# Optimization experiments

Measured on AMD Instinct MI355X. Metric: run time of the kernel, lower is better.

The kernel has to match this reference:

```python
import jax, jax.numpy as jnp
import numpy as np

B, H, M, DH = 8, 32, 8, 64  # batch, spatial h=w, heads, dim_head
C = M * DH
HW = H * H


def _make_pos_idx(h: int) -> np.ndarray:
    # A[i, j] = j - i, matching tf.constant([range(i, i+h) for i in range(0, -h, -1)])
    A = np.arange(h)[None, :] - np.arange(h)[:, None]
    horiz = np.tile(A, (h, h))                              # (h^2, h^2)
    vert = np.repeat(np.repeat(A, h, axis=0), h, axis=1)    # (h^2, h^2)
    return (2 * h - 1) * (vert + h - 1) + (horiz + h - 1)   # values in [0, (2h-1)^2)


def setup_inputs() -> dict:
    key = jax.random.key(0)
    ks = jax.random.split(key, 4)
    x = jax.random.normal(ks[0], (B, H, H, C), dtype=jnp.float32)
    w_qkv = jax.random.normal(ks[1], (DH, 3 * DH), dtype=jnp.float32) * (1.0 / np.sqrt(DH))
    b_qkv = jnp.zeros((3 * DH,), dtype=jnp.float32)
    w_ht = jax.random.normal(ks[2], (C, C), dtype=jnp.float32) * (1.0 / np.sqrt(C))
    b_ht = jnp.zeros((C,), dtype=jnp.float32)
    # Glorot-normal scalar table over (2h-1)^2 relative positions
    n_rel = (2 * H - 1) ** 2
    pos_table = jax.random.normal(ks[3], (n_rel,), dtype=jnp.float32) * np.float32(np.sqrt(2.0 / (n_rel + 1)))
    pos_idx = jnp.asarray(_make_pos_idx(H), dtype=jnp.int32)  # (HW, HW)
    return {"x": x, "w_qkv": w_qkv, "b_qkv": b_qkv, "w_ht": w_ht, "b_ht": b_ht,
            "pos_table": pos_table, "pos_idx": pos_idx}


def reference(x, w_qkv, b_qkv, w_ht, b_ht, pos_table, pos_idx):
    b, h, w, c = x.shape
    d_h = c // M
    # split heads into the batch dim: (b*M, h, w, d_h)
    xh = x.reshape(b, h, w, M, d_h).transpose(0, 3, 1, 2, 4).reshape(b * M, h, w, d_h)
    # 1x1 conv == per-pixel dense
    qkv = xh @ w_qkv + b_qkv                       # (b*M, h, w, 3*DH)
    qkv = qkv.reshape(b * M, h * w, DH, 3)
    q, k, v = qkv[..., 0], qkv[..., 1], qkv[..., 2]
    q = q / jnp.sqrt(jnp.float32(DH))
    att = jnp.einsum('bic,bjc->bij', q, k)         # (b*M, HW, HW)
    pos_emb = pos_table[pos_idx]                   # (HW, HW) gathered bias
    att = jax.nn.softmax(att + pos_emb, axis=-1)
    o = jnp.einsum('bij,bjc->bic', att, v)         # (b*M, HW, DH)
    o = o.reshape(b, M, h, w, d_h).transpose(0, 2, 3, 1, 4).reshape(b, h, w, c)
    out = o @ w_ht + b_ht                          # 1x1 head_transform conv
    return (out, att, pos_emb)
```

## Files before the change

kernel.cpp:

```cpp
#include <hip/hip_runtime.h>
#include <hip/hip_bf16.h>

typedef __attribute__((ext_vector_type(8))) __bf16 bf16x8;
typedef __attribute__((ext_vector_type(8))) short  s16x8;
typedef __attribute__((ext_vector_type(4))) short  s16x4;
typedef __attribute__((ext_vector_type(4))) float  f32x4;

#define HW2 1024
#define CDIM 512

static __device__ __forceinline__ unsigned short f2b(float f) {
  __hip_bfloat16 h = __float2bfloat16(f);
  return __builtin_bit_cast(unsigned short, h);
}

static __device__ __forceinline__ f32x4 mfma16(s16x8 a, s16x8 b, f32x4 c) {
  return __builtin_amdgcn_mfma_f32_16x16x32_bf16(
      __builtin_bit_cast(bf16x8, a), __builtin_bit_cast(bf16x8, b), c, 0, 0, 0);
}

static __device__ __forceinline__ void lds_fence() {
  asm volatile("s_waitcnt lgkmcnt(0)" ::: "memory");
  __builtin_amdgcn_sched_barrier(0);
}

__global__ __launch_bounds__(256) void k_prep(
    const float* __restrict__ w_qkv, const float* __restrict__ w_ht,
    const float* __restrict__ table, const int* __restrict__ idx,
    unsigned short* __restrict__ Wtq, unsigned short* __restrict__ Wtk,
    unsigned short* __restrict__ Wtv, unsigned short* __restrict__ WhtT,
    float* __restrict__ pe) {
  int blk = blockIdx.x;
  if (blk < 16) {
    int i = blk * 256 + threadIdx.x;
    int c = i >> 6, k = i & 63;
    const float* src = w_qkv + k * 192 + 3 * c;
    Wtq[i] = f2b(src[0] * 0.125f);
    Wtk[i] = f2b(src[1]);
    Wtv[i] = f2b(src[2]);
  } else if (blk < 1040) {
    int i = (blk - 16) * 256 + threadIdx.x;
    int c = i >> 9, k = i & 511;
    WhtT[i] = f2b(w_ht[k * 512 + c]);
  } else {
    int i = (blk - 1040) * 256 + threadIdx.x;
    #pragma unroll
    for (int j = 0; j < 4; ++j) {
      int p = i + j * 262144;
      pe[p] = table[idx[p]];
    }
  }
}

__global__ __launch_bounds__(256) void k_qkv(const float* __restrict__ x,
    const float* __restrict__ b_qkv,
    const unsigned short* __restrict__ Wtq, const unsigned short* __restrict__ Wtk,
    const unsigned short* __restrict__ Wtv,
    unsigned short* __restrict__ Qb, unsigned short* __restrict__ Kb,
    unsigned short* __restrict__ Vt) {
  int bm = blockIdx.x >> 4;
  int pt = blockIdx.x & 15;
  int wid = threadIdx.x >> 6, lane = threadIdx.x & 63;
  int l15 = lane & 15, lg = lane >> 4;
  int b = bm >> 3, m = bm & 7;
  int pbase = pt * 64 + wid * 16;

  int pA = pbase + l15;
  const float* xp = x + (size_t)(b * HW2 + pA) * CDIM + m * 64 + lg * 8;
  f32x4 xv0 = *(const f32x4*)(xp);
  f32x4 xv1 = *(const f32x4*)(xp + 4);
  f32x4 xv2 = *(const f32x4*)(xp + 32);
  f32x4 xv3 = *(const f32x4*)(xp + 36);
  s16x8 a0, a1;
  #pragma unroll
  for (int j = 0; j < 4; ++j) {
    a0[j]     = (short)f2b(xv0[j]);
    a0[4 + j] = (short)f2b(xv1[j]);
    a1[j]     = (short)f2b(xv2[j]);
    a1[4 + j] = (short)f2b(xv3[j]);
  }

  f32x4 acc[12];
  #pragma unroll
  for (int ct = 0; ct < 12; ++ct) acc[ct] = (f32x4){0.f, 0.f, 0.f, 0.f};

  #pragma unroll
  for (int ct = 0; ct < 12; ++ct) {
    const unsigned short* W = (ct < 4) ? Wtq : (ct < 8 ? Wtk : Wtv);
    int c = (ct & 3) * 16 + l15;
    const unsigned short* wp = W + c * 64 + lg * 8;
    s16x8 b0 = *(const s16x8*)(wp);
    s16x8 b1 = *(const s16x8*)(wp + 32);
    if (ct < 8) {
      acc[ct] = mfma16(b0, a0, acc[ct]);
      acc[ct] = mfma16(b1, a1, acc[ct]);
    } else {
      acc[ct] = mfma16(a0, b0, acc[ct]);
      acc[ct] = mfma16(a1, b1, acc[ct]);
    }
  }

  #pragma unroll
  for (int ct = 0; ct < 8; ++ct) {
    int s = ct >> 2;
    int c0 = (ct & 3) * 16 + lg * 4;
    unsigned short* D = (s == 0) ? Qb : Kb;
    s16x4 pk;
    #pragma unroll
    for (int i = 0; i < 4; ++i) {
      float bias = b_qkv[3 * (c0 + i) + s];
      if (s == 0) bias *= 0.125f;
      pk[i] = (short)f2b(acc[ct][i] + bias);
    }
    *(s16x4*)(D + (size_t)(bm * HW2 + pbase + l15) * 64 + c0) = pk;
  }
  #pragma unroll
  for (int ct = 8; ct < 12; ++ct) {
    int c = (ct & 3) * 16 + l15;
    float bias = b_qkv[3 * c + 2];
    s16x4 pk;
    #pragma unroll
    for (int i = 0; i < 4; ++i) pk[i] = (short)f2b(acc[ct][i] + bias);
    *(s16x4*)(Vt + ((size_t)bm * 64 + c) * HW2 + pbase + lg * 4) = pk;
  }
}

__global__ __launch_bounds__(256, 4) void k_attn(
    const unsigned short* __restrict__ Qb, const unsigned short* __restrict__ Kb,
    const unsigned short* __restrict__ Vt, const float* __restrict__ ptab,
    float* __restrict__ att, unsigned short* __restrict__ O) {
  int r8 = blockIdx.x & 7;
  int kk = blockIdx.x >> 3;
  int qt = kk & 63;
  int bm = ((kk >> 6) << 3) | r8;
  int wid = threadIdx.x >> 6, lane = threadIdx.x & 63;
  int l15 = lane & 15, lg = lane >> 4;

  __shared__ __align__(16) unsigned char buf[16 * 1032 * 2];
  __shared__ float redm[4][16];
  __shared__ float reds[4][16];
  unsigned short (*P)[1032] = (unsigned short(*)[1032])buf;

  const unsigned short* qp = Qb + (size_t)(bm * HW2 + qt * 16 + l15) * 64 + lg * 8;
  s16x8 qa0 = *(const s16x8*)qp;
  s16x8 qa1 = *(const s16x8*)(qp + 32);

  f32x4 acc[16];
  const unsigned short* kbase = Kb + (size_t)bm * HW2 * 64;
  #pragma unroll
  for (int ct = 0; ct < 16; ++ct) {
    int col = wid * 256 + ct * 16 + l15;
    const unsigned short* kp = kbase + (size_t)col * 64 + lg * 8;
    s16x8 kb0 = *(const s16x8*)kp;
    s16x8 kb1 = *(const s16x8*)(kp + 32);
    f32x4 a = (f32x4){0.f, 0.f, 0.f, 0.f};
    a = mfma16(kb0, qa0, a);
    a = mfma16(kb1, qa1, a);
    acc[ct] = a;
  }

  int cb = 1984 - 63 * (qt >> 1) - ((qt & 1) << 4) - l15;
  float pm = -1e30f;
  #pragma unroll
  for (int ct = 0; ct < 16; ++ct) {
    int c0 = wid * 256 + ct * 16 + lg * 4;
    int t0 = 63 * (c0 >> 5) + (c0 & 31) + cb;
    f32x4 pv;
    __builtin_memcpy(&pv, ptab + t0, 16);
    #pragma unroll
    for (int i = 0; i < 4; ++i) {
      float v = acc[ct][i] + pv[i];
      acc[ct][i] = v;
      pm = fmaxf(pm, v);
    }
  }
  pm = fmaxf(pm, __shfl_xor(pm, 16));
  pm = fmaxf(pm, __shfl_xor(pm, 32));
  if (lane < 16) redm[wid][l15] = pm;
  __syncthreads();
  float mrow = fmaxf(fmaxf(redm[0][l15], redm[1][l15]),
                     fmaxf(redm[2][l15], redm[3][l15]));

  float ps = 0.f;
  #pragma unroll
  for (int ct = 0; ct < 16; ++ct) {
    #pragma unroll
    for (int i = 0; i < 4; ++i) {
      float e = __expf(acc[ct][i] - mrow);
      acc[ct][i] = e;
      ps += e;
    }
  }
  ps += __shfl_xor(ps, 16);
  ps += __shfl_xor(ps, 32);
  if (lane < 16) reds[wid][l15] = ps;
  __syncthreads();
  float inv = 1.0f / (reds[0][l15] + reds[1][l15] + reds[2][l15] + reds[3][l15]);

  #pragma unroll
  for (int ct = 0; ct < 16; ++ct) {
    int c0 = wid * 256 + ct * 16 + lg * 4;
    s16x4 pk;
    #pragma unroll
    for (int i = 0; i < 4; ++i) {
      float v = acc[ct][i] * inv;
      acc[ct][i] = v;
      pk[i] = (short)f2b(v);
    }
    *(s16x4*)&P[l15][c0] = pk;
  }
  __syncthreads();

  f32x4 o = (f32x4){0.f, 0.f, 0.f, 0.f};
  const unsigned short* vbase = Vt + (size_t)(bm * 64 + wid * 16 + l15) * HW2;
  #pragma unroll
  for (int kt = 0; kt < 32; ++kt) {
    s16x8 vb = *(const s16x8*)(vbase + kt * 32 + lg * 8);
    s16x8 pa = *(const s16x8*)&P[l15][kt * 32 + lg * 8];
    o = mfma16(vb, pa, o);
  }
  s16x4 ok;
  #pragma unroll
  for (int i = 0; i < 4; ++i) ok[i] = (short)f2b(o[i]);
  *(s16x4*)(O + (size_t)(bm * HW2 + qt * 16 + l15) * 64 + wid * 16 + lg * 4) = ok;

  __syncthreads();

  float* stgw = (float*)buf + wid * 1024;
  float* abase = att + (size_t)(bm * HW2 + qt * 16) * HW2 + wid * 256;
  #pragma unroll
  for (int q = 0; q < 4; ++q) {
    #pragma unroll
    for (int t4 = 0; t4 < 4; ++t4) {
      int ct = q * 4 + t4;
      f32x4 vv;
      #pragma unroll
      for (int i = 0; i < 4; ++i) vv[i] = acc[ct][i];
      int cw = (t4 * 4 + lg) ^ (l15 & 7);
      *(f32x4*)&stgw[l15 * 64 + cw * 4] = vv;
    }
    lds_fence();
    f32x4 vals[4];
    #pragma unroll
    for (int i = 0; i < 4; ++i) {
      int r = i * 4 + lg;
      int cr = l15 ^ (r & 7);
      vals[i] = *(const f32x4*)&stgw[r * 64 + cr * 4];
    }
    lds_fence();
    #pragma unroll
    for (int i = 0; i < 4; ++i) {
      int r = i * 4 + lg;
      __builtin_nontemporal_store(vals[i],
          (f32x4*)(abase + (size_t)r * HW2 + q * 64 + l15 * 4));
    }
  }
}

__global__ __launch_bounds__(256) void k_ht(
    const unsigned short* __restrict__ O, const unsigned short* __restrict__ WhtT,
    const float* __restrict__ b_ht, float* __restrict__ out) {
  int rt = blockIdx.x >> 1;
  int ch = blockIdx.x & 1;
  int wid = threadIdx.x >> 6, lane = threadIdx.x & 63;
  int wr = wid >> 1, wc = wid & 1;
  int l15 = lane & 15, lg = lane >> 4;
  int b = (rt * 32) >> 10;
  int p0 = (rt * 32) & 1023;

  __shared__ unsigned short A[32][520];

  int t = threadIdx.x;
  #pragma unroll
  for (int j = 0; j < 8; ++j) {
    int idx = t * 8 + j * 2048;
    int row = idx >> 9;
    int k0 = idx & 511;
    int m = k0 >> 6, kk = k0 & 63;
    const unsigned short* src = O + (size_t)((b * 8 + m) * HW2 + p0 + row) * 64 + kk;
    *(s16x8*)&A[row][k0] = *(const s16x8*)src;
  }
  __syncthreads();

  f32x4 acc[8];
  #pragma unroll
  for (int ct = 0; ct < 8; ++ct) acc[ct] = (f32x4){0.f, 0.f, 0.f, 0.f};

  #pragma unroll
  for (int kt = 0; kt < 16; ++kt) {
    s16x8 a = *(const s16x8*)&A[wr * 16 + l15][kt * 32 + lg * 8];
    #pragma unroll
    for (int ct = 0; ct < 8; ++ct) {
      int col = ch * 256 + wc * 128 + ct * 16 + l15;
      s16x8 bf = *(const s16x8*)(WhtT + (size_t)col * 512 + kt * 32 + lg * 8);
      acc[ct] = mfma16(bf, a, acc[ct]);
    }
  }

  int rp = rt * 32 + wr * 16 + l15;
  #pragma unroll
  for (int ct = 0; ct < 8; ++ct) {
    int c0 = ch * 256 + wc * 128 + ct * 16 + lg * 4;
    f32x4 bb = *(const f32x4*)(b_ht + c0);
    f32x4 ov;
    #pragma unroll
    for (int i = 0; i < 4; ++i) ov[i] = acc[ct][i] + bb[i];
    *(f32x4*)(out + (size_t)rp * 512 + c0) = ov;
  }
}

extern "C" void kernel_launch(void* const* d_in, const int* in_sizes, int n_in,
                              void* d_out, int out_size, void* d_ws, size_t ws_size,
                              hipStream_t stream) {
  const float* x         = (const float*)d_in[0];
  const float* w_qkv     = (const float*)d_in[1];
  const float* b_qkv     = (const float*)d_in[2];
  const float* w_ht      = (const float*)d_in[3];
  const float* b_ht      = (const float*)d_in[4];
  const float* pos_table = (const float*)d_in[5];
  const int*   pos_idx   = (const int*)d_in[6];

  float* out = (float*)d_out;
  float* att = out + 4194304;
  float* pe  = att + 67108864;

  char* ws = (char*)d_ws;
  unsigned short* Qb   = (unsigned short*)(ws);
  unsigned short* Kb   = (unsigned short*)(ws + (8u  << 20));
  unsigned short* Vt   = (unsigned short*)(ws + (16u << 20));
  unsigned short* O    = (unsigned short*)(ws + (24u << 20));
  unsigned short* Wtq  = (unsigned short*)(ws + (32u << 20));
  unsigned short* Wtk  = Wtq + 4096;
  unsigned short* Wtv  = Wtk + 4096;
  unsigned short* WhtT = (unsigned short*)(ws + (32u << 20) + 65536);

  k_prep<<<2064, 256, 0, stream>>>(w_qkv, w_ht, pos_table, pos_idx,
                                   Wtq, Wtk, Wtv, WhtT, pe);
  k_qkv <<<1024, 256, 0, stream>>>(x, b_qkv, Wtq, Wtk, Wtv, Qb, Kb, Vt);
  k_attn<<<4096, 256, 0, stream>>>(Qb, Kb, Vt, pos_table, att, O);
  k_ht  <<<512,  256, 0, stream>>>(O, WhtT, b_ht, out);
}
```

Measured before the change: 203.9 us.

## Fuse attention and head-transform into one kernel with per-wave heads and two-pass softmax

```diff
diff --git a/kernel.cpp b/kernel.cpp
--- a/kernel.cpp
+++ b/kernel.cpp
@@ -125,187 +125,175 @@
   }
 }
 
-__global__ __launch_bounds__(256, 4) void k_attn(
+__global__ __launch_bounds__(512, 4) void k_fused(
     const unsigned short* __restrict__ Qb, const unsigned short* __restrict__ Kb,
     const unsigned short* __restrict__ Vt, const float* __restrict__ ptab,
-    float* __restrict__ att, unsigned short* __restrict__ O) {
-  int r8 = blockIdx.x & 7;
-  int kk = blockIdx.x >> 3;
-  int qt = kk & 63;
-  int bm = ((kk >> 6) << 3) | r8;
+    const unsigned short* __restrict__ WhtT, const float* __restrict__ b_ht,
+    float* __restrict__ att, float* __restrict__ out) {
+  int b  = blockIdx.x & 7;
+  int qt = blockIdx.x >> 3;
   int wid = threadIdx.x >> 6, lane = threadIdx.x & 63;
   int l15 = lane & 15, lg = lane >> 4;
-
-  __shared__ __align__(16) unsigned char buf[16 * 1032 * 2];
-  __shared__ float redm[4][16];
-  __shared__ float reds[4][16];
-  unsigned short (*P)[1032] = (unsigned short(*)[1032])buf;
+  int bm = b * 8 + wid;
+
+  __shared__ __align__(16) unsigned char wbuf[8][4352];
+  __shared__ unsigned short Osm[16][520];
 
   const unsigned short* qp = Qb + (size_t)(bm * HW2 + qt * 16 + l15) * 64 + lg * 8;
   s16x8 qa0 = *(const s16x8*)qp;
   s16x8 qa1 = *(const s16x8*)(qp + 32);
-
-  f32x4 acc[16];
   const unsigned short* kbase = Kb + (size_t)bm * HW2 * 64;
-  #pragma unroll
-  for (int ct = 0; ct < 16; ++ct) {
-    int col = wid * 256 + ct * 16 + l15;
-    const unsigned short* kp = kbase + (size_t)col * 64 + lg * 8;
-    s16x8 kb0 = *(const s16x8*)kp;
-    s16x8 kb1 = *(const s16x8*)(kp + 32);
-    f32x4 a = (f32x4){0.f, 0.f, 0.f, 0.f};
-    a = mfma16(kb0, qa0, a);
-    a = mfma16(kb1, qa1, a);
-    acc[ct] = a;
-  }
-
   int cb = 1984 - 63 * (qt >> 1) - ((qt & 1) << 4) - l15;
-  float pm = -1e30f;
-  #pragma unroll
-  for (int ct = 0; ct < 16; ++ct) {
-    int c0 = wid * 256 + ct * 16 + lg * 4;
-    int t0 = 63 * (c0 >> 5) + (c0 & 31) + cb;
-    f32x4 pv;
-    __builtin_memcpy(&pv, ptab + t0, 16);
-    #pragma unroll
-    for (int i = 0; i < 4; ++i) {
-      float v = acc[ct][i] + pv[i];
-      acc[ct][i] = v;
-      pm = fmaxf(pm, v);
-    }
-  }
-  pm = fmaxf(pm, __shfl_xor(pm, 16));
-  pm = fmaxf(pm, __shfl_xor(pm, 32));
-  if (lane < 16) redm[wid][l15] = pm;
+
+  float mrow = -1e30f, srow = 0.f;
+  for (int ch = 0; ch < 8; ++ch) {
+    f32x4 acc[8];
+    #pragma unroll
+    for (int ct = 0; ct < 8; ++ct) {
+      int col = ch * 128 + ct * 16 + l15;
+      const unsigned short* kp = kbase + (size_t)col * 64 + lg * 8;
+      s16x8 kb0 = *(const s16x8*)kp;
+      s16x8 kb1 = *(const s16x8*)(kp + 32);
+      f32x4 a = (f32x4){0.f, 0.f, 0.f, 0.f};
+      a = mfma16(kb0, qa0, a);
+      a = mfma16(kb1, qa1, a);
+      acc[ct] = a;
+    }
+    float cm = -1e30f;
+    #pragma unroll
+    for (int ct = 0; ct < 8; ++ct) {
+      int c0 = ch * 128 + ct * 16 + lg * 4;
+      int t0 = 63 * (c0 >> 5) + (c0 & 31) + cb;
+      f32x4 pv;
+      __builtin_memcpy(&pv, ptab + t0, 16);
+      #pragma unroll
+      for (int i = 0; i < 4; ++i) {
+        float v = acc[ct][i] + pv[i];
+        acc[ct][i] = v;
+        cm = fmaxf(cm, v);
+      }
+    }
+    cm = fmaxf(cm, __shfl_xor(cm, 16));
+    cm = fmaxf(cm, __shfl_xor(cm, 32));
+    float mn = fmaxf(mrow, cm);
+    float cs = 0.f;
+    #pragma unroll
+    for (int ct = 0; ct < 8; ++ct)
+      #pragma unroll
+      for (int i = 0; i < 4; ++i) cs += __expf(acc[ct][i] - mn);
+    cs += __shfl_xor(cs, 16);
+    cs += __shfl_xor(cs, 32);
+    srow = srow * __expf(mrow - mn) + cs;
+    mrow = mn;
+  }
+  float inv = 1.0f / srow;
+
+  float* stgw = (float*)&wbuf[wid][0];
+  unsigned short* Pw = (unsigned short*)&wbuf[wid][0];
+  float* abase = att + (size_t)(bm * HW2 + qt * 16) * HW2;
+  f32x4 o[4];
+  #pragma unroll
+  for (int d = 0; d < 4; ++d) o[d] = (f32x4){0.f, 0.f, 0.f, 0.f};
+
+  for (int ch = 0; ch < 8; ++ch) {
+    f32x4 acc[8];
+    #pragma unroll
+    for (int ct = 0; ct < 8; ++ct) {
+      int col = ch * 128 + ct * 16 + l15;
+      const unsigned short* kp = kbase + (size_t)col * 64 + lg * 8;
+      s16x8 kb0 = *(const s16x8*)kp;
+      s16x8 kb1 = *(const s16x8*)(kp + 32);
+      f32x4 a = (f32x4){0.f, 0.f, 0.f, 0.f};
+      a = mfma16(kb0, qa0, a);
+      a = mfma16(kb1, qa1, a);
+      acc[ct] = a;
+    }
+    #pragma unroll
+    for (int ct = 0; ct < 8; ++ct) {
+      int c0 = ch * 128 + ct * 16 + lg * 4;
+      int t0 = 63 * (c0 >> 5) + (c0 & 31) + cb;
+      f32x4 pv;
+      __builtin_memcpy(&pv, ptab + t0, 16);
+      #pragma unroll
+      for (int i = 0; i < 4; ++i)
+        acc[ct][i] = __expf(acc[ct][i] + pv[i] - mrow) * inv;
+    }
+    #pragma unroll
+    for (int q = 0; q < 2; ++q) {
+      #pragma unroll
+      for (int t4 = 0; t4 < 4; ++t4) {
+        int cw = (t4 * 4 + lg) ^ (l15 & 7);
+        *(f32x4*)&stgw[l15 * 64 + cw * 4] = acc[q * 4 + t4];
+      }
+      lds_fence();
+      f32x4 vals[4];
+      #pragma unroll
+      for (int i = 0; i < 4; ++i) {
+        int r = i * 4 + lg;
+        int cr = l15 ^ (r & 7);
+        vals[i] = *(const f32x4*)&stgw[r * 64 + cr * 4];
+      }
+      lds_fence();
+      #pragma unroll
+      for (int i = 0; i < 4; ++i) {
+        int r = i * 4 + lg;
+        __builtin_nontemporal_store(vals[i],
+            (f32x4*)(abase + (size_t)r * HW2 + ch * 128 + q * 64 + l15 * 4));
+      }
+    }
+    #pragma unroll
+    for (int ct = 0; ct < 8; ++ct) {
+      int c = ct * 16 + lg * 4;
+      s16x4 pk;
+      #pragma unroll
+      for (int i = 0; i < 4; ++i) pk[i] = (short)f2b(acc[ct][i]);
+      *(s16x4*)&Pw[l15 * 136 + c] = pk;
+    }
+    lds_fence();
+    #pragma unroll
+    for (int d = 0; d < 4; ++d) {
+      const unsigned short* vp =
+          Vt + (size_t)(bm * 64 + d * 16 + l15) * HW2 + ch * 128;
+      #pragma unroll
+      for (int kt = 0; kt < 4; ++kt) {
+        s16x8 vb = *(const s16x8*)(vp + kt * 32 + lg * 8);
+        s16x8 pa = *(const s16x8*)&Pw[l15 * 136 + kt * 32 + lg * 8];
+        o[d] = mfma16(vb, pa, o[d]);
+      }
+    }
+    lds_fence();
+  }
+
+  #pragma unroll
+  for (int d = 0; d < 4; ++d) {
+    s16x4 ok;
+    #pragma unroll
+    for (int i = 0; i < 4; ++i) ok[i] = (short)f2b(o[d][i]);
+    *(s16x4*)&Osm[l15][wid * 64 + d * 16 + lg * 4] = ok;
+  }
   __syncthreads();
-  float mrow = fmaxf(fmaxf(redm[0][l15], redm[1][l15]),
-                     fmaxf(redm[2][l15], redm[3][l15]));
-
-  float ps = 0.f;
-  #pragma unroll
-  for (int ct = 0; ct < 16; ++ct) {
-    #pragma unroll
-    for (int i = 0; i < 4; ++i) {
-      float e = __expf(acc[ct][i] - mrow);
-      acc[ct][i] = e;
-      ps += e;
-    }
-  }
-  ps += __shfl_xor(ps, 16);
-  ps += __shfl_xor(ps, 32);
-  if (lane < 16) reds[wid][l15] = ps;
-  __syncthreads();
-  float inv = 1.0f / (reds[0][l15] + reds[1][l15] + reds[2][l15] + reds[3][l15]);
-
-  #pragma unroll
-  for (int ct = 0; ct < 16; ++ct) {
-    int c0 = wid * 256 + ct * 16 + lg * 4;
-    s16x4 pk;
-    #pragma unroll
-    for (int i = 0; i < 4; ++i) {
-      float v = acc[ct][i] * inv;
-      acc[ct][i] = v;
-      pk[i] = (short)f2b(v);
-    }
-    *(s16x4*)&P[l15][c0] = pk;
-  }
-  __syncthreads();
-
-  f32x4 o = (f32x4){0.f, 0.f, 0.f, 0.f};
-  const unsigned short* vbase = Vt + (size_t)(bm * 64 + wid * 16 + l15) * HW2;
-  #pragma unroll
-  for (int kt = 0; kt < 32; ++kt) {
-    s16x8 vb = *(const s16x8*)(vbase + kt * 32 + lg * 8);
-    s16x8 pa = *(const s16x8*)&P[l15][kt * 32 + lg * 8];
-    o = mfma16(vb, pa, o);
-  }
-  s16x4 ok;
-  #pragma unroll
-  for (int i = 0; i < 4; ++i) ok[i] = (short)f2b(o[i]);
-  *(s16x4*)(O + (size_t)(bm * HW2 + qt * 16 + l15) * 64 + wid * 16 + lg * 4) = ok;
-
-  __syncthreads();
-
-  float* stgw = (float*)buf + wid * 1024;
-  float* abase = att + (size_t)(bm * HW2 + qt * 16) * HW2 + wid * 256;
-  #pragma unroll
-  for (int q = 0; q < 4; ++q) {
-    #pragma unroll
-    for (int t4 = 0; t4 < 4; ++t4) {
-      int ct = q * 4 + t4;
-      f32x4 vv;
-      #pragma unroll
-      for (int i = 0; i < 4; ++i) vv[i] = acc[ct][i];
-      int cw = (t4 * 4 + lg) ^ (l15 & 7);
-      *(f32x4*)&stgw[l15 * 64 + cw * 4] = vv;
-    }
-    lds_fence();
-    f32x4 vals[4];
-    #pragma unroll
-    for (int i = 0; i < 4; ++i) {
-      int r = i * 4 + lg;
-      int cr = l15 ^ (r & 7);
-      vals[i] = *(const f32x4*)&stgw[r * 64 + cr * 4];
-    }
-    lds_fence();
-    #pragma unroll
-    for (int i = 0; i < 4; ++i) {
-      int r = i * 4 + lg;
-      __builtin_nontemporal_store(vals[i],
-          (f32x4*)(abase + (size_t)r * HW2 + q * 64 + l15 * 4));
-    }
-  }
-}
-
-__global__ __launch_bounds__(256) void k_ht(
-    const unsigned short* __restrict__ O, const unsigned short* __restrict__ WhtT,
-    const float* __restrict__ b_ht, float* __restrict__ out) {
-  int rt = blockIdx.x >> 1;
-  int ch = blockIdx.x & 1;
-  int wid = threadIdx.x >> 6, lane = threadIdx.x & 63;
-  int wr = wid >> 1, wc = wid & 1;
-  int l15 = lane & 15, lg = lane >> 4;
-  int b = (rt * 32) >> 10;
-  int p0 = (rt * 32) & 1023;
-
-  __shared__ unsigned short A[32][520];
-
-  int t = threadIdx.x;
-  #pragma unroll
-  for (int j = 0; j < 8; ++j) {
-    int idx = t * 8 + j * 2048;
-    int row = idx >> 9;
-    int k0 = idx & 511;
-    int m = k0 >> 6, kk = k0 & 63;
-    const unsigned short* src = O + (size_t)((b * 8 + m) * HW2 + p0 + row) * 64 + kk;
-    *(s16x8*)&A[row][k0] = *(const s16x8*)src;
-  }
-  __syncthreads();
-
-  f32x4 acc[8];
-  #pragma unroll
-  for (int ct = 0; ct < 8; ++ct) acc[ct] = (f32x4){0.f, 0.f, 0.f, 0.f};
-
+
+  f32x4 ah[4];
+  #pragma unroll
+  for (int ct = 0; ct < 4; ++ct) ah[ct] = (f32x4){0.f, 0.f, 0.f, 0.f};
   #pragma unroll
   for (int kt = 0; kt < 16; ++kt) {
-    s16x8 a = *(const s16x8*)&A[wr * 16 + l15][kt * 32 + lg * 8];
-    #pragma unroll
-    for (int ct = 0; ct < 8; ++ct) {
-      int col = ch * 256 + wc * 128 + ct * 16 + l15;
+    s16x8 oa = *(const s16x8*)&Osm[l15][kt * 32 + lg * 8];
+    #pragma unroll
+    for (int ct = 0; ct < 4; ++ct) {
+      int col = wid * 64 + ct * 16 + l15;
       s16x8 bf = *(const s16x8*)(WhtT + (size_t)col * 512 + kt * 32 + lg * 8);
-      acc[ct] = mfma16(bf, a, acc[ct]);
-    }
-  }
-
-  int rp = rt * 32 + wr * 16 + l15;
-  #pragma unroll
-  for (int ct = 0; ct < 8; ++ct) {
-    int c0 = ch * 256 + wc * 128 + ct * 16 + lg * 4;
+      ah[ct] = mfma16(bf, oa, ah[ct]);
+    }
+  }
+  #pragma unroll
+  for (int ct = 0; ct < 4; ++ct) {
+    int c0 = wid * 64 + ct * 16 + lg * 4;
     f32x4 bb = *(const f32x4*)(b_ht + c0);
     f32x4 ov;
     #pragma unroll
-    for (int i = 0; i < 4; ++i) ov[i] = acc[ct][i] + bb[i];
-    *(f32x4*)(out + (size_t)rp * 512 + c0) = ov;
+    for (int i = 0; i < 4; ++i) ov[i] = ah[ct][i] + bb[i];
+    *(f32x4*)(out + (size_t)(b * HW2 + qt * 16 + l15) * 512 + c0) = ov;
   }
 }
 
@@ -328,15 +316,13 @@
   unsigned short* Qb   = (unsigned short*)(ws);
   unsigned short* Kb   = (unsigned short*)(ws + (8u  << 20));
   unsigned short* Vt   = (unsigned short*)(ws + (16u << 20));
-  unsigned short* O    = (unsigned short*)(ws + (24u << 20));
   unsigned short* Wtq  = (unsigned short*)(ws + (32u << 20));
   unsigned short* Wtk  = Wtq + 4096;
   unsigned short* Wtv  = Wtk + 4096;
   unsigned short* WhtT = (unsigned short*)(ws + (32u << 20) + 65536);
 
-  k_prep<<<2064, 256, 0, stream>>>(w_qkv, w_ht, pos_table, pos_idx,
-                                   Wtq, Wtk, Wtv, WhtT, pe);
-  k_qkv <<<1024, 256, 0, stream>>>(x, b_qkv, Wtq, Wtk, Wtv, Qb, Kb, Vt);
-  k_attn<<<4096, 256, 0, stream>>>(Qb, Kb, Vt, pos_table, att, O);
-  k_ht  <<<512,  256, 0, stream>>>(O, WhtT, b_ht, out);
-}
+  k_prep <<<2064, 256, 0, stream>>>(w_qkv, w_ht, pos_table, pos_idx,
+                                    Wtq, Wtk, Wtv, WhtT, pe);
+  k_qkv  <<<1024, 256, 0, stream>>>(x, b_qkv, Wtq, Wtk, Wtv, Qb, Kb, Vt);
+  k_fused<<<512,  512, 0, stream>>>(Qb, Kb, Vt, pos_table, WhtT, b_ht, att, out);
+}
```

Measured after the change: 263.1 us. +29.0%, slower.
